# Optimization experiments

Hardware: AMD Instinct MI355X
Metric: run time of the kernel (lower is better)

The kernel has to match this reference:

```python
import jax, jax.numpy as jnp
import numpy as np

C, N, G = 10, 500000, 8


def setup_inputs() -> dict:
    key = jax.random.key(0)
    k1, k2 = jax.random.split(key)
    group_act = jax.random.uniform(k1, (C, N, G), dtype=jnp.float32)
    target_labels = jax.random.randint(k2, (N,), 0, 11, dtype=jnp.int64 if jax.config.jax_enable_x64 else jnp.int32)
    return {"group_act": group_act, "target_labels": target_labels}


def reference(group_act, target_labels):
    # group_act: [C, N, G] (stacked list_group_activation), target_labels: [N] in 0..C (0 => ignored)
    labels = target_labels.reshape(-1) - 1                      # [N], -1 => skip
    c, n, g = group_act.shape
    masks = (labels[None, :] == jnp.arange(c)[:, None]).astype(group_act.dtype)  # [C, N]
    counts = masks.sum(axis=1)                                  # [C]
    valid = counts >= 2                                         # classes actually contributing

    Am = group_act * masks[:, :, None]                          # [C, N, G] masked activations
    col_sum = Am.sum(axis=1)                                    # [C, G]
    p = Am / col_sum[:, None, :]                                # normalized per column (zero on unmasked rows)
    # log only over masked rows (original indexes rows by cls_mask before log)
    m3 = masks[:, :, None] > 0
    logp = jnp.where(m3, jnp.log(jnp.where(m3, p, 1.0)), 0.0)   # [C, N, G]

    # M[c, i, j] = sum_n p[c,n,i] * log p[c,n,j]; loss_ij = -M[c,i,j] for i != j
    M = jnp.einsum('cni,cnj->cij', p, logp)                     # [C, G, G]
    offdiag = M * (1.0 - jnp.eye(g, dtype=M.dtype))
    per_class = offdiag.sum(axis=(1, 2))                        # [C]

    num = jnp.sum(jnp.where(valid, per_class, 0.0))
    denom = jnp.sum(valid.astype(M.dtype)) * (g * (g - 1))
    # original: tot = mean(-M_ij); return -tot == mean(M_ij)
    return num / denom
```

## Files before the change

kernel.cpp:

```cpp
#include <hip/hip_runtime.h>

#define C_CLS 10
#define G_DIM 8
#define CHUNKS 128
#define ACC_W 25

__device__ inline float wave_red(float v) {
#pragma unroll
    for (int off = 32; off > 0; off >>= 1) v += __shfl_down(v, off, 64);
    return v;
}

__global__ void __launch_bounds__(256) k_main(const float* __restrict__ ga,
                                              const int* __restrict__ lbl,
                                              float* __restrict__ part, int N) {
    const int c = blockIdx.y;
    const int chunk_len = (N + CHUNKS - 1) / CHUNKS;
    const int base = blockIdx.x * chunk_len;
    const int end = min(base + chunk_len, N);

    float cs_a[G_DIM] = {0,0,0,0,0,0,0,0};
    float R_a[G_DIM]  = {0,0,0,0,0,0,0,0};
    float D_a[G_DIM]  = {0,0,0,0,0,0,0,0};
    float cnt = 0.0f;

    const float* plane = ga + (size_t)c * N * G_DIM;
    for (int n = base + (int)threadIdx.x; n < end; n += blockDim.x) {
        if (lbl[n] == c + 1) {
            const float4* row = (const float4*)(plane + (size_t)n * G_DIM);
            float4 v0 = row[0];
            float4 v1 = row[1];
            float a[G_DIM] = {v0.x, v0.y, v0.z, v0.w, v1.x, v1.y, v1.z, v1.w};
            float la[G_DIM];
            float L = 0.0f;
#pragma unroll
            for (int g = 0; g < G_DIM; ++g) {
                la[g] = __logf(fmaxf(a[g], 1e-30f));
                L += la[g];
            }
            cnt += 1.0f;
#pragma unroll
            for (int g = 0; g < G_DIM; ++g) {
                cs_a[g] += a[g];
                R_a[g] = fmaf(a[g], L, R_a[g]);
                D_a[g] = fmaf(a[g], la[g], D_a[g]);
            }
        }
    }

#pragma unroll
    for (int g = 0; g < G_DIM; ++g) {
        cs_a[g] = wave_red(cs_a[g]);
        R_a[g]  = wave_red(R_a[g]);
        D_a[g]  = wave_red(D_a[g]);
    }
    cnt = wave_red(cnt);

    __shared__ float s_part[4][ACC_W];
    int wid = threadIdx.x >> 6, lid = threadIdx.x & 63;
    if (lid == 0) {
#pragma unroll
        for (int g = 0; g < G_DIM; ++g) {
            s_part[wid][g]      = cs_a[g];
            s_part[wid][8 + g]  = R_a[g];
            s_part[wid][16 + g] = D_a[g];
        }
        s_part[wid][24] = cnt;
    }
    __syncthreads();
    int t = threadIdx.x;
    if (t < ACC_W) {
        float v = s_part[0][t] + s_part[1][t] + s_part[2][t] + s_part[3][t];
        part[((size_t)c * CHUNKS + blockIdx.x) * ACC_W + t] = v;
    }
}

__global__ void k_fin(const float* __restrict__ part, float* __restrict__ out) {
    __shared__ float s_acc[C_CLS][ACC_W];
    int t = threadIdx.x;
    if (t < C_CLS * ACC_W) {
        int c = t / ACC_W, j = t % ACC_W;
        float s = 0.0f;
        for (int ch = 0; ch < CHUNKS; ++ch)
            s += part[((size_t)c * CHUNKS + ch) * ACC_W + j];
        s_acc[c][j] = s;
    }
    __syncthreads();
    if (t == 0) {
        float tot = 0.0f;
        int nv = 0;
        for (int c = 0; c < C_CLS; ++c) {
            if (s_acc[c][24] >= 2.0f) {
                nv++;
                float K = 0.0f, s = 0.0f;
                for (int i = 0; i < G_DIM; ++i) {
                    float cs = s_acc[c][i];
                    K += __logf(cs);
                    s += (s_acc[c][8 + i] - s_acc[c][16 + i]) / cs;
                }
                tot += s - (float)(G_DIM - 1) * K;
            }
        }
        out[0] = tot / ((float)nv * (float)(G_DIM * (G_DIM - 1)));
    }
}

extern "C" void kernel_launch(void* const* d_in, const int* in_sizes, int n_in,
                              void* d_out, int out_size, void* d_ws, size_t ws_size,
                              hipStream_t stream) {
    const float* ga = (const float*)d_in[0];
    const int* lbl = (const int*)d_in[1];
    float* out = (float*)d_out;
    int N = in_sizes[1];

    float* part = (float*)d_ws;

    dim3 grid(CHUNKS, C_CLS);
    k_main<<<grid, 256, 0, stream>>>(ga, lbl, part, N);
    k_fin<<<1, 256, 0, stream>>>(part, out);
}
```

Baseline: 224.5 us.

## Read each label once and scatter per-class sums via shared-memory atomics

Replaces the class-by-chunk grid, where every class block scanned the whole label array, with a single grid-stride pass. Each row's label picks its class, and only that class plane is read. Per-row contributions go into a per-block shared-memory accumulator through atomics, then into striped global accumulators that a final kernel sums. This removes the tenfold label reads and the idle threads on non-matching rows, but adds heavy shared-memory atomic contention (25 atomics per row over only 10 classes), a memset, and nondeterministic float summation order.

```diff
diff --git a/kernel.cpp b/kernel.cpp
--- a/kernel.cpp
+++ b/kernel.cpp
@@ -2,103 +2,71 @@
 
 #define C_CLS 10
 #define G_DIM 8
-#define CHUNKS 128
-#define ACC_W 25
-
-__device__ inline float wave_red(float v) {
-#pragma unroll
-    for (int off = 32; off > 0; off >>= 1) v += __shfl_down(v, off, 64);
-    return v;
-}
+#define NACC 25
+#define NTOT (C_CLS * NACC)
+#define NSTRIPE 16
 
 __global__ void __launch_bounds__(256) k_main(const float* __restrict__ ga,
                                               const int* __restrict__ lbl,
-                                              float* __restrict__ part, int N) {
-    const int c = blockIdx.y;
-    const int chunk_len = (N + CHUNKS - 1) / CHUNKS;
-    const int base = blockIdx.x * chunk_len;
-    const int end = min(base + chunk_len, N);
+                                              float* __restrict__ acc, int N) {
+    __shared__ float s_acc[NTOT];
+    for (int t = threadIdx.x; t < NTOT; t += 256) s_acc[t] = 0.0f;
+    __syncthreads();
 
-    float cs_a[G_DIM] = {0,0,0,0,0,0,0,0};
-    float R_a[G_DIM]  = {0,0,0,0,0,0,0,0};
-    float D_a[G_DIM]  = {0,0,0,0,0,0,0,0};
-    float cnt = 0.0f;
-
-    const float* plane = ga + (size_t)c * N * G_DIM;
-    for (int n = base + (int)threadIdx.x; n < end; n += blockDim.x) {
-        if (lbl[n] == c + 1) {
-            const float4* row = (const float4*)(plane + (size_t)n * G_DIM);
-            float4 v0 = row[0];
-            float4 v1 = row[1];
+    const int T = gridDim.x * blockDim.x;
+    for (int n = blockIdx.x * 256 + threadIdx.x; n < N; n += T) {
+        const int c = lbl[n] - 1;
+        if (c >= 0) {
+            const float4* row = (const float4*)(ga + ((size_t)c * N + n) * G_DIM);
+            const float4 v0 = row[0];
+            const float4 v1 = row[1];
             float a[G_DIM] = {v0.x, v0.y, v0.z, v0.w, v1.x, v1.y, v1.z, v1.w};
-            float la[G_DIM];
-            float L = 0.0f;
+            float la[G_DIM], L = 0.0f;
 #pragma unroll
             for (int g = 0; g < G_DIM; ++g) {
                 la[g] = __logf(fmaxf(a[g], 1e-30f));
                 L += la[g];
             }
-            cnt += 1.0f;
+            float* sa = s_acc + c * NACC;
 #pragma unroll
             for (int g = 0; g < G_DIM; ++g) {
-                cs_a[g] += a[g];
-                R_a[g] = fmaf(a[g], L, R_a[g]);
-                D_a[g] = fmaf(a[g], la[g], D_a[g]);
+                atomicAdd(&sa[g],      a[g]);
+                atomicAdd(&sa[8 + g],  a[g] * L);
+                atomicAdd(&sa[16 + g], a[g] * la[g]);
             }
+            atomicAdd(&sa[24], 1.0f);
         }
     }
 
-#pragma unroll
-    for (int g = 0; g < G_DIM; ++g) {
-        cs_a[g] = wave_red(cs_a[g]);
-        R_a[g]  = wave_red(R_a[g]);
-        D_a[g]  = wave_red(D_a[g]);
-    }
-    cnt = wave_red(cnt);
-
-    __shared__ float s_part[4][ACC_W];
-    int wid = threadIdx.x >> 6, lid = threadIdx.x & 63;
-    if (lid == 0) {
-#pragma unroll
-        for (int g = 0; g < G_DIM; ++g) {
-            s_part[wid][g]      = cs_a[g];
-            s_part[wid][8 + g]  = R_a[g];
-            s_part[wid][16 + g] = D_a[g];
-        }
-        s_part[wid][24] = cnt;
-    }
     __syncthreads();
-    int t = threadIdx.x;
-    if (t < ACC_W) {
-        float v = s_part[0][t] + s_part[1][t] + s_part[2][t] + s_part[3][t];
-        part[((size_t)c * CHUNKS + blockIdx.x) * ACC_W + t] = v;
-    }
+    const int stripe = blockIdx.x & (NSTRIPE - 1);
+    for (int t = threadIdx.x; t < NTOT; t += 256)
+        atomicAdd(&acc[stripe * NTOT + t], s_acc[t]);
 }
 
-__global__ void k_fin(const float* __restrict__ part, float* __restrict__ out) {
-    __shared__ float s_acc[C_CLS][ACC_W];
-    int t = threadIdx.x;
-    if (t < C_CLS * ACC_W) {
-        int c = t / ACC_W, j = t % ACC_W;
-        float s = 0.0f;
-        for (int ch = 0; ch < CHUNKS; ++ch)
-            s += part[((size_t)c * CHUNKS + ch) * ACC_W + j];
-        s_acc[c][j] = s;
+__global__ void k_fin(const float* __restrict__ acc, float* __restrict__ out) {
+    __shared__ float s[NTOT];
+    const int t = threadIdx.x;
+    if (t < NTOT) {
+        float v = 0.0f;
+        for (int r = 0; r < NSTRIPE; ++r) v += acc[r * NTOT + t];
+        s[t] = v;
     }
     __syncthreads();
     if (t == 0) {
         float tot = 0.0f;
         int nv = 0;
         for (int c = 0; c < C_CLS; ++c) {
-            if (s_acc[c][24] >= 2.0f) {
+            const float* sa = s + c * NACC;
+            if (sa[24] >= 2.0f) {
                 nv++;
-                float K = 0.0f, s = 0.0f;
+                float K = 0.0f, ss = 0.0f;
                 for (int i = 0; i < G_DIM; ++i) {
-                    float cs = s_acc[c][i];
+                    float cs = sa[i];
                     K += __logf(cs);
-                    s += (s_acc[c][8 + i] - s_acc[c][16 + i]) / cs;
+                    ss += (sa[8 + i] - sa[16 + i]) / cs;
                 }
-                tot += s - (float)(G_DIM - 1) * K;
+                tot += ss - (float)(G_DIM - 1) * K;
             }
         }
         out[0] = tot / ((float)nv * (float)(G_DIM * (G_DIM - 1)));
@@ -111,11 +79,14 @@
     const float* ga = (const float*)d_in[0];
     const int* lbl = (const int*)d_in[1];
     float* out = (float*)d_out;
-    int N = in_sizes[1];
+    const int N = in_sizes[1];
 
-    float* part = (float*)d_ws;
+    float* acc = (float*)d_ws;
 
-    dim3 grid(CHUNKS, C_CLS);
-    k_main<<<grid, 256, 0, stream>>>(ga, lbl, part, N);
-    k_fin<<<1, 256, 0, stream>>>(part, out);
+    hipMemsetAsync(acc, 0, NSTRIPE * NTOT * sizeof(float), stream);
+
+    int blocks = (N + 255) / 256;
+    if (blocks > 8192) blocks = 8192;
+    k_main<<<blocks, 256, 0, stream>>>(ga, lbl, acc, N);
+    k_fin<<<1, 256, 0, stream>>>(acc, out);
 }
```

Result: slower. 254.1 us (+13.2%).

## Compress labels to bytes in a pre-pass and process four rows per thread

Applied to the files above, without the earlier changes.

Adds a kernel that packs the int32 labels into a uint8 array in workspace. The main kernel then reads four labels per thread as one uchar4 and loops over the four rows, which cuts the label traffic that every class plane re-reads. The cost is an extra launch plus a write and read of the byte array. Each thread now handles four strided rows per step, so row reads inside a wave become less coalesced.

```diff
diff --git a/kernel.cpp b/kernel.cpp
--- a/kernel.cpp
+++ b/kernel.cpp
@@ -11,11 +11,28 @@
     return v;
 }
 
+__global__ void __launch_bounds__(256) k_lbl(const int* __restrict__ lbl,
+                                             unsigned char* __restrict__ lbl8, int N) {
+    const int i = blockIdx.x * blockDim.x + threadIdx.x;
+    const int n4 = i * 4;
+    if (n4 + 3 < N) {
+        int4 v = ((const int4*)lbl)[i];
+        uchar4 u;
+        u.x = (unsigned char)v.x; u.y = (unsigned char)v.y;
+        u.z = (unsigned char)v.z; u.w = (unsigned char)v.w;
+        ((uchar4*)lbl8)[i] = u;
+    } else if (n4 < N) {
+        for (int k = 0; k < 4 && n4 + k < N; ++k)
+            lbl8[n4 + k] = (unsigned char)lbl[n4 + k];
+    }
+}
+
 __global__ void __launch_bounds__(256) k_main(const float* __restrict__ ga,
-                                              const int* __restrict__ lbl,
+                                              const unsigned char* __restrict__ lbl8,
                                               float* __restrict__ part, int N) {
     const int c = blockIdx.y;
-    const int chunk_len = (N + CHUNKS - 1) / CHUNKS;
+    const unsigned char cc = (unsigned char)(c + 1);
+    const int chunk_len = (((N + CHUNKS - 1) / CHUNKS) + 3) & ~3;
     const int base = blockIdx.x * chunk_len;
     const int end = min(base + chunk_len, N);
 
@@ -25,25 +42,31 @@
     float cnt = 0.0f;
 
     const float* plane = ga + (size_t)c * N * G_DIM;
-    for (int n = base + (int)threadIdx.x; n < end; n += blockDim.x) {
-        if (lbl[n] == c + 1) {
-            const float4* row = (const float4*)(plane + (size_t)n * G_DIM);
-            float4 v0 = row[0];
-            float4 v1 = row[1];
-            float a[G_DIM] = {v0.x, v0.y, v0.z, v0.w, v1.x, v1.y, v1.z, v1.w};
-            float la[G_DIM];
-            float L = 0.0f;
+
+    for (int n4 = base + (int)threadIdx.x * 4; n4 < end; n4 += 256 * 4) {
+        const uchar4 lv = *(const uchar4*)(lbl8 + n4);
+        const unsigned char l[4] = {lv.x, lv.y, lv.z, lv.w};
 #pragma unroll
-            for (int g = 0; g < G_DIM; ++g) {
-                la[g] = __logf(fmaxf(a[g], 1e-30f));
-                L += la[g];
-            }
-            cnt += 1.0f;
+        for (int k = 0; k < 4; ++k) {
+            const int n = n4 + k;
+            if (n < end && l[k] == cc) {
+                const float4* row = (const float4*)(plane + (size_t)n * G_DIM);
+                const float4 v0 = row[0];
+                const float4 v1 = row[1];
+                float a[G_DIM] = {v0.x, v0.y, v0.z, v0.w, v1.x, v1.y, v1.z, v1.w};
+                float la[G_DIM], L = 0.0f;
 #pragma unroll
-            for (int g = 0; g < G_DIM; ++g) {
-                cs_a[g] += a[g];
-                R_a[g] = fmaf(a[g], L, R_a[g]);
-                D_a[g] = fmaf(a[g], la[g], D_a[g]);
+                for (int g = 0; g < G_DIM; ++g) {
+                    la[g] = __logf(fmaxf(a[g], 1e-30f));
+                    L += la[g];
+                }
+                cnt += 1.0f;
+#pragma unroll
+                for (int g = 0; g < G_DIM; ++g) {
+                    cs_a[g] += a[g];
+                    R_a[g] = fmaf(a[g], L, R_a[g]);
+                    D_a[g] = fmaf(a[g], la[g], D_a[g]);
+                }
             }
         }
     }
@@ -57,7 +80,7 @@
     cnt = wave_red(cnt);
 
     __shared__ float s_part[4][ACC_W];
-    int wid = threadIdx.x >> 6, lid = threadIdx.x & 63;
+    const int wid = threadIdx.x >> 6, lid = threadIdx.x & 63;
     if (lid == 0) {
 #pragma unroll
         for (int g = 0; g < G_DIM; ++g) {
@@ -68,7 +91,7 @@
         s_part[wid][24] = cnt;
     }
     __syncthreads();
-    int t = threadIdx.x;
+    const int t = threadIdx.x;
     if (t < ACC_W) {
         float v = s_part[0][t] + s_part[1][t] + s_part[2][t] + s_part[3][t];
         part[((size_t)c * CHUNKS + blockIdx.x) * ACC_W + t] = v;
@@ -77,9 +100,9 @@
 
 __global__ void k_fin(const float* __restrict__ part, float* __restrict__ out) {
     __shared__ float s_acc[C_CLS][ACC_W];
-    int t = threadIdx.x;
+    const int t = threadIdx.x;
     if (t < C_CLS * ACC_W) {
-        int c = t / ACC_W, j = t % ACC_W;
+        const int c = t / ACC_W, j = t % ACC_W;
         float s = 0.0f;
         for (int ch = 0; ch < CHUNKS; ++ch)
             s += part[((size_t)c * CHUNKS + ch) * ACC_W + j];
@@ -111,11 +134,15 @@
     const float* ga = (const float*)d_in[0];
     const int* lbl = (const int*)d_in[1];
     float* out = (float*)d_out;
-    int N = in_sizes[1];
+    const int N = in_sizes[1];
 
     float* part = (float*)d_ws;
+    unsigned char* lbl8 = (unsigned char*)d_ws + 128 * 1024;
+
+    const int lblocks = (N + 1023) / 1024;
+    k_lbl<<<lblocks, 256, 0, stream>>>(lbl, lbl8, N);
 
     dim3 grid(CHUNKS, C_CLS);
-    k_main<<<grid, 256, 0, stream>>>(ga, lbl, part, N);
+    k_main<<<grid, 256, 0, stream>>>(ga, lbl8, part, N);
     k_fin<<<1, 256, 0, stream>>>(part, out);
 }
```

New measurement: 220.6 us. About the same (-1.7%).
